# Optimization experiments

Measured on AMD Instinct MI355X. Metric: run time of the kernel, lower is better.

## Reference

```python
import jax, jax.numpy as jnp
import numpy as np

NUM_ELEMENTS = 14
EMPTY_ID, WALL_ID = 0, 1
# 8-neighborhood direction offsets (dy, dx); DIRS[(a+4)%8] == -DIRS[a]
DIRS = [(-1, 0), (-1, 1), (0, 1), (1, 1), (1, 0), (1, -1), (0, -1), (-1, -1)]


def shift(x, a):
    """out[..., i, j] = x[..., i+dy, j+dx] with zero padding at borders (pw.direction_func)."""
    dy, dx = DIRS[a]
    B, C, H, W = x.shape
    xp = jnp.pad(x, ((0, 0), (0, 0), (1, 1), (1, 1)))
    return jax.lax.slice(xp, (0, 0, 1 + dy, 1 + dx), (B, C, 1 + dy + H, 1 + dx + W))


def setup_inputs() -> dict:
    key = jax.random.key(0)
    k1, k2 = jax.random.split(key)
    B, C, H, W = 4, NUM_ELEMENTS + 6, 512, 512
    world = jax.random.uniform(k1, (B, C, H, W), dtype=jnp.float32)
    velocity_field = jax.random.normal(k2, (B, 2, H, W), dtype=jnp.float32)
    elem_empty = jnp.zeros((C,), dtype=jnp.float32).at[EMPTY_ID].set(1.0)
    return {"world": world, "velocity_field": velocity_field, "elem_empty": elem_empty}


def reference(world, velocity_field, elem_empty):
    dtype = world.dtype
    empty_vec = elem_empty[None, :, None, None]  # [1, C, 1, 1]
    inv_2pi = 1.0 / (2.0 * np.pi)

    for _ in range(2):
        mag = jnp.linalg.norm(velocity_field, axis=1, keepdims=True)  # [B,1,H,W]
        raw = inv_2pi * jnp.arccos(velocity_field[:, 1:2] / (mag + 0.001))
        ang = jnp.where(velocity_field[:, 0:1] < 0, 1.0 - raw, raw)
        bucket = jnp.mod(jnp.floor(ang * 8.0 + 0.5), 8.0)
        vel_enough = mag > 0.1
        vdelta = velocity_field
        for a in range(8):
            opp = (a + 4) % 8
            empty_b = world[:, EMPTY_ID:EMPTY_ID + 1] > 0.5
            wall_b = world[:, WALL_ID:WALL_ID + 1] > 0.5
            is_match = bucket == a
            is_empty_dir = shift(empty_b, a) & (~wall_b)
            sa = is_match & vel_enough & is_empty_dir          # does_become_empty
            sb = shift(sa, opp)                                 # does_become_opposite
            saf = sa.astype(dtype)
            sbf = sb.astype(dtype)
            opp_world = shift(world, opp)
            # interp_vel: world - sa*world - sb*world + sa*empty_vec + sb*opp_world
            world = world - saf * world - sbf * world + saf * empty_vec + sbf * opp_world
            opp_vel = shift(velocity_field, opp)
            vdelta = vdelta - saf * velocity_field * 0.5 + sbf * opp_vel * 0.5
        velocity_field = vdelta

    velocity_field = velocity_field * 0.95
    kernel = jnp.ones((1, 1, 3, 3), dtype) / 18.0

    def smooth(ch):  # ch: [B,1,H,W]
        conv = jax.lax.conv_general_dilated(
            ch, kernel, window_strides=(1, 1), padding=((1, 1), (1, 1)),
            dimension_numbers=("NCHW", "OIHW", "NCHW"))
        return conv + ch * 0.5

    velocity_field = jnp.concatenate(
        [smooth(velocity_field[:, 0:1]), smooth(velocity_field[:, 1:2])], axis=1)
    world = world.at[:, NUM_ELEMENTS + 4:NUM_ELEMENTS + 6].set(velocity_field)
    return world, velocity_field
```

## Files before the change

### kernel.cpp

```cpp
#include <hip/hip_runtime.h>
#include <math.h>

#define HH 512
#define WW 512
#define HW (HH*WW)
#define BATCH 4
#define NCH 18
#define BHW (BATCH*HW)

__device__ __constant__ int cDG[8] = {-512,-511,1,513,512,511,-1,-513};
__device__ __constant__ int cDT[8] = {-48,-47,1,49,48,47,-1,-49};

__global__ __launch_bounds__(256) void bv_bucket_kernel(
    const float* __restrict__ vel, unsigned char* __restrict__ bk,
    unsigned* __restrict__ pcount)
{
    int idx = blockIdx.x*256 + threadIdx.x;
    if (idx == 0) { pcount[0] = 0; pcount[1] = 0; }
    if (idx >= BHW) return;
    int b = idx >> 18;
    int rem = idx & (HW-1);
    const float* vb = vel + (size_t)b*2*HW;
    float vy = vb[rem];
    float vx = vb[HW + rem];
    float a2 = vy*vy;
    float b2 = vx*vx;
    float mag = sqrtf(a2 + b2);
    float xx = vx / (mag + 0.001f);
    float af = (float)acos((double)xx);
    const float inv2pi = (float)(1.0/(2.0*3.14159265358979323846));
    float raw = inv2pi * af;
    float ang = (vy < 0.0f) ? (1.0f - raw) : raw;
    float t = ang * 8.0f + 0.5f;
    int bkt = (int)floorf(t);
    bkt &= 7;
    unsigned char e = (mag > 0.1f) ? (unsigned char)8 : (unsigned char)0;
    bk[idx] = (unsigned char)(bkt | e);
}

#define ATP 48
#define ATC (48*48)
#define ANT 512
#define PAD 49

template<bool COMPOSE>
__global__ __launch_bounds__(ANT) void bv_mask_kernel(
    const float* __restrict__ Win, int Cin,
    float* __restrict__ Wout, int Cout,
    const unsigned char* __restrict__ bkall,
    unsigned char* __restrict__ Mg,
    unsigned char* __restrict__ SBg,
    int* __restrict__ SrcOut,
    const int* __restrict__ Src1g,
    unsigned* __restrict__ pcount,
    uint2* __restrict__ tlist,
    unsigned listcap,
    const float* __restrict__ elem_empty)
{
    __shared__ __align__(16) unsigned char SHM[40864];
    float* A0  = ((float*)(SHM +     0)) + PAD;
    float* A1  = ((float*)(SHM +  9608)) + PAD;
    float* B0F = ((float*)(SHM + 19216)) + PAD;
    float* B1F = ((float*)(SHM + 28824)) + PAD;
    unsigned char* KSH = SHM + 38432 + PAD;
    unsigned* sCnt = (unsigned*)(SHM + 40840);

    unsigned char* MSHb = SHM + 19216 + PAD;
    unsigned char* SBb  = SHM + 28824 + PAD;

    const int tid = threadIdx.x;
    const int blk = blockIdx.x;
    const int tx = blk & 15, ty = (blk >> 4) & 15, b = blk >> 8;
    const int x0 = tx*32 - 8, y0 = ty*32 - 8;

    const float* inb  = Win  + (size_t)b*Cin*HW;
    float*       outb = Wout + (size_t)b*Cout*HW;
    const unsigned char* bkb = bkall + ((size_t)b << 18);
    unsigned char* Mob  = Mg  + ((size_t)b << 18);
    unsigned char* SBob = SBg + ((size_t)b << 18);
    int*           Srb  = SrcOut + ((size_t)b << 18);

    const float e0 = elem_empty[0];
    const float e1 = elem_empty[1];

    float v0r[4], v1r[4];
    unsigned kreg[4], mreg[4];
    unsigned mtail = 0;

    if (tid == 0) sCnt[0] = 0;

    #pragma unroll
    for (int k = 0; k < 4; ++k) {
        int l = tid + (k << 9);
        int ly = l / ATP, lx = l - ly*ATP;
        int gy = y0 + ly, gx = x0 + lx;
        bool in = ((unsigned)gy < HH) && ((unsigned)gx < WW);
        int g = gy*WW + gx;
        float v0 = 0.f, v1 = 0.f; unsigned char kk = 0;
        if (in) { v0 = inb[g]; v1 = inb[HW + g]; kk = bkb[g]; }
        A0[l] = v0; A1[l] = v1; KSH[l] = kk;
        v0r[k] = v0; v1r[k] = v1; kreg[k] = kk; mreg[k] = 0;
    }
    if (tid < 256) {
        int l = 2048 + tid;
        int ly = l / ATP, lx = l - ly*ATP;
        int gy = y0 + ly, gx = x0 + lx;
        bool in = ((unsigned)gy < HH) && ((unsigned)gx < WW);
        int g = gy*WW + gx;
        float v0 = 0.f, v1 = 0.f; unsigned char kk = 0;
        if (in) { v0 = inb[g]; v1 = inb[HW + g]; kk = bkb[g]; }
        A0[l] = v0; A1[l] = v1; KSH[l] = kk;
    }
    __syncthreads();

    #pragma unroll
    for (int a = 0; a < 8; ++a) {
        const int doff = cDT[a];
        const unsigned tgt = (unsigned)(a | 8);
        const float* cA0 = (a & 1) ? B0F : A0;
        const float* cA1 = (a & 1) ? B1F : A1;
        float* nA0 = (a & 1) ? A0 : B0F;
        float* nA1 = (a & 1) ? A1 : B1F;
        #pragma unroll
        for (int k = 0; k < 4; ++k) {
            const int l = tid + (k << 9);
            const int ln = l + doff;
            const int lo = l - doff;
            float a0l = v0r[k], a1l = v1r[k];
            float a0n = cA0[ln];
            float a0o = cA0[lo], a1o = cA1[lo];
            unsigned ko = KSH[lo];
            bool sal = ((kreg[k] & 15u) == tgt) & (a0n > 0.5f) & !(a1l > 0.5f);
            bool sao = ((ko & 15u) == tgt) & (a0l > 0.5f) & !(a1o > 0.5f);
            mreg[k] |= (sal ? 1u : 0u) << a;
            float sa = sal ? 1.0f : 0.0f;
            float sb = sao ? 1.0f : 0.0f;
            float r0 = a0l - sa*a0l; r0 = r0 - sb*a0l; r0 = r0 + sa*e0; r0 = r0 + sb*a0o;
            float r1 = a1l - sa*a1l; r1 = r1 - sb*a1l; r1 = r1 + sa*e1; r1 = r1 + sb*a1o;
            v0r[k] = r0; v1r[k] = r1;
            nA0[l] = r0; nA1[l] = r1;
        }
        if (tid < 256) {
            const int l = 2048 + tid;
            const int ln = l + doff;
            const int lo = l - doff;
            float a0l = cA0[l], a1l = cA1[l];
            float a0n = cA0[ln];
            float a0o = cA0[lo], a1o = cA1[lo];
            unsigned kl = KSH[l], ko = KSH[lo];
            bool sal = ((kl & 15u) == tgt) & (a0n > 0.5f) & !(a1l > 0.5f);
            bool sao = ((ko & 15u) == tgt) & (a0l > 0.5f) & !(a1o > 0.5f);
            if (sal) mtail |= 1u << a;
            float sa = sal ? 1.0f : 0.0f;
            float sb = sao ? 1.0f : 0.0f;
            float r0 = a0l - sa*a0l; r0 = r0 - sb*a0l; r0 = r0 + sa*e0; r0 = r0 + sb*a0o;
            float r1 = a1l - sa*a1l; r1 = r1 - sb*a1l; r1 = r1 + sa*e1; r1 = r1 + sb*a1o;
            nA0[l] = r0; nA1[l] = r1;
        }
        __syncthreads();
    }

    #pragma unroll
    for (int k = 0; k < 4; ++k) MSHb[tid + (k << 9)] = (unsigned char)mreg[k];
    if (tid < 256) MSHb[2048 + tid] = (unsigned char)mtail;
    __syncthreads();

    for (int l = tid; l < ATC; l += ANT) {
        unsigned sb8 = 0;
        #pragma unroll
        for (int a = 0; a < 8; ++a) {
            int lo = l - cDT[a];
            sb8 |= (unsigned)((MSHb[lo] >> a) & 1) << a;
        }
        SBb[l] = (unsigned char)sb8;
    }
    __syncthreads();

    int tNeed[2]; unsigned tLL[2], tEy[2];
    #pragma unroll
    for (int it = 0; it < 2; ++it) {
        tNeed[it] = 0;
        int li = tid + (it << 9);
        int iy = li >> 5, ix = li & 31;
        int l = (iy + 8)*ATP + ix + 8;
        int gy = ty*32 + iy, gx = tx*32 + ix;
        int g = gy*WW + gx;
        outb[g]      = A0[l];
        outb[HW + g] = A1[l];
        unsigned mm = MSHb[l], sbb = SBb[l];
        Mob[g]  = (unsigned char)mm;
        SBob[g] = (unsigned char)sbb;

        int cc = l, ss = 7, kd = 0;
        unsigned m = mm, sb = sbb;
        while (true) {
            unsigned evt = (m | sb) & ((2u << ss) - 1u);
            if (!evt) { kd = 0; break; }
            int bb = 31 - __builtin_clz(evt);
            int ia = (m >> bb) & 1, ib = (sb >> bb) & 1;
            if (ia && ib) { kd = 2; break; }
            if (ia) { kd = 1; break; }
            cc -= cDT[bb]; ss = bb - 1;
            if (ss < 0) { kd = 0; break; }
            m = MSHb[cc]; sb = SBb[cc];
        }
        if (kd == 1) {
            Srb[g] = (int)(1u << 30);
        } else if (kd == 0) {
            int cly = cc / ATP, clx = cc - cly*ATP;
            unsigned s = (unsigned)((y0 + cly)*WW + (x0 + clx));
            if (!COMPOSE) {
                Srb[g] = (int)s;
            } else {
                unsigned r1 = (unsigned)Src1g[((size_t)b << 18) + s];
                unsigned k1 = r1 >> 30;
                if (k1 == 0u)      Srb[g] = (int)r1;
                else if (k1 == 1u) Srb[g] = (int)(1u << 30);
                else { tNeed[it] = 1; tEy[it] = s; }
            }
        } else {
            if (!COMPOSE) {
                Srb[g] = (int)(2u << 30);
            } else {
                int cly = cc / ATP, clx = cc - cly*ATP;
                unsigned ccg = (unsigned)((y0 + cly)*WW + (x0 + clx));
                tNeed[it] = 1;
                tEy[it] = (1u << 31) | ((unsigned)ss << 28) | ccg;
            }
        }
        if (COMPOSE && tNeed[it]) tLL[it] = atomicAdd(&sCnt[0], 1u);
    }
    if constexpr (COMPOSE) {
        __syncthreads();
        if (tid == 0) sCnt[1] = sCnt[0] ? atomicAdd(&pcount[1], sCnt[0]) : 0u;
        __syncthreads();
        unsigned lbase = sCnt[1];
        #pragma unroll
        for (int it = 0; it < 2; ++it) {
            if (!tNeed[it]) continue;
            int li = tid + (it << 9);
            int iy = li >> 5, ix = li & 31;
            int g = (ty*32 + iy)*WW + tx*32 + ix;
            unsigned lidx = lbase + tLL[it];
            if (lidx < listcap) {
                tlist[lidx] = make_uint2(((unsigned)b << 18) | (unsigned)g, tEy[it]);
                Srb[g] = (int)(2u << 30);
            } else {
                Srb[g] = (int)(3u << 30);
            }
        }
    }
}

__global__ __launch_bounds__(256) void bv_vdelta_kernel(
    const unsigned char* __restrict__ M,
    const unsigned char* __restrict__ SB,
    const float* __restrict__ vel,
    float* __restrict__ vdout,
    unsigned char* __restrict__ bkout,
    unsigned* __restrict__ pcount)
{
    int idx = blockIdx.x*256 + threadIdx.x;
    if (bkout && idx == 0) pcount[1] = 0;
    if (idx >= BHW) return;
    int b = idx >> 18;
    int g = idx & (HW-1);
    const float* velb = vel   + (size_t)b*2*HW;
    float*       vdb  = vdout + (size_t)b*2*HW;
    unsigned mm  = M[((size_t)b << 18) + g];
    unsigned sbb = SB[((size_t)b << 18) + g];
    float vy = velb[g], vx = velb[HW + g];
    float ddy = vy, ddx = vx;
    unsigned act = mm | sbb;
    if (act) {
        #pragma unroll
        for (int a = 0; a < 8; ++a) {
            if ((act >> a) & 1) {
                float sa = (float)((mm  >> a) & 1);
                float sb = (float)((sbb >> a) & 1);
                float voy = 0.f, vox = 0.f;
                if (sb != 0.f) {
                    int go = g - cDG[a];
                    voy = velb[go]; vox = velb[HW + go];
                }
                ddy = ddy - (sa*vy)*0.5f; ddy = ddy + (sb*voy)*0.5f;
                ddx = ddx - (sa*vx)*0.5f; ddx = ddx + (sb*vox)*0.5f;
            }
        }
    }
    vdb[g]      = ddy;
    vdb[HW + g] = ddx;
    if (bkout) {
        float a2 = ddy*ddy;
        float b2 = ddx*ddx;
        float mag = sqrtf(a2 + b2);
        float xx = ddx / (mag + 0.001f);
        float af = (float)acos((double)xx);
        const float inv2pi = (float)(1.0/(2.0*3.14159265358979323846));
        float raw = inv2pi * af;
        float ang = (ddy < 0.0f) ? (1.0f - raw) : raw;
        float t = ang * 8.0f + 0.5f;
        int bkt = (int)floorf(t);
        bkt &= 7;
        unsigned char e = (mag > 0.1f) ? (unsigned char)8 : (unsigned char)0;
        bkout[idx] = (unsigned char)(bkt | e);
    }
}

__device__ __attribute__((noinline)) float bv_eval(
    int cell, int stp,
    const unsigned char* __restrict__ M,
    const unsigned char* __restrict__ SB,
    const float* __restrict__ initc)
{
    float vstk[10]; int vsp = 0;
    int cs_cell[10], cs_stp[10], cs_ph[10]; int csp = 0;
    cs_cell[0] = cell; cs_stp[0] = stp; cs_ph[0] = 0; csp = 1;
    while (csp > 0) {
        int ph = cs_ph[csp-1];
        if (ph == 0) {
            int cc = cs_cell[csp-1], ss = cs_stp[csp-1];
            float result = 0.0f; int have = 0;
            while (true) {
                if (ss < 0) { result = initc[cc]; have = 1; break; }
                unsigned m = M[cc], sb = SB[cc];
                unsigned evt = (m | sb) & ((2u << ss) - 1u);
                if (!evt) { result = initc[cc]; have = 1; break; }
                int bb = 31 - __builtin_clz(evt);
                int ia = (m >> bb) & 1, ib = (sb >> bb) & 1;
                if (ia && ib) {
                    cs_cell[csp-1] = cc; cs_stp[csp-1] = bb; cs_ph[csp-1] = 1;
                    cs_cell[csp] = cc - cDG[bb]; cs_stp[csp] = bb - 1; cs_ph[csp] = 0; csp++;
                    break;
                }
                if (ia) { result = 0.0f; have = 1; break; }
                cc -= cDG[bb]; ss = bb - 1;
            }
            if (have) { vstk[vsp++] = result; csp--; }
        } else if (ph == 1) {
            cs_ph[csp-1] = 2;
            cs_cell[csp] = cs_cell[csp-1]; cs_stp[csp] = cs_stp[csp-1] - 1;
            cs_ph[csp] = 0; csp++;
        } else {
            float Bv = vstk[--vsp]; float Av = vstk[--vsp];
            vstk[vsp++] = Av - Bv;
            csp--;
        }
    }
    return vstk[0];
}

__device__ float bv_leaf1_1(int L,
    const unsigned char* __restrict__ M1,
    const unsigned char* __restrict__ SB1,
    const float* __restrict__ ic)
{
    int cc = L, ss = 7;
    while (true) {
        unsigned m = M1[cc], sb = SB1[cc];
        unsigned evt = (m | sb) & ((2u << ss) - 1u);
        if (!evt) break;
        int bb = 31 - __builtin_clz(evt);
        int ia = (m >> bb) & 1, ib = (sb >> bb) & 1;
        if (ia && ib) return bv_eval(cc, bb, M1, SB1, ic);
        if (ia) return 0.0f;
        cc -= cDG[bb]; ss = bb - 1;
        if (ss < 0) break;
    }
    return ic[cc];
}

__device__ float bv_eval1_ind(int cell, int stp,
    const unsigned char* __restrict__ M2,
    const unsigned char* __restrict__ SB2,
    const unsigned char* __restrict__ M1,
    const unsigned char* __restrict__ SB1,
    const float* __restrict__ ic)
{
    float vstk[10]; int vsp = 0;
    int cs_cell[10], cs_stp[10], cs_ph[10]; int csp = 0;
    cs_cell[0] = cell; cs_stp[0] = stp; cs_ph[0] = 0; csp = 1;
    while (csp > 0) {
        int ph = cs_ph[csp-1];
        if (ph == 0) {
            int cc = cs_cell[csp-1], ss = cs_stp[csp-1];
            int have = 0, zero = 0, leaf = 0;
            while (true) {
                if (ss < 0) { leaf = cc; have = 1; break; }
                unsigned m = M2[cc], sb = SB2[cc];
                unsigned evt = (m | sb) & ((2u << ss) - 1u);
                if (!evt) { leaf = cc; have = 1; break; }
                int bb = 31 - __builtin_clz(evt);
                int ia = (m >> bb) & 1, ib = (sb >> bb) & 1;
                if (ia && ib) {
                    cs_cell[csp-1] = cc; cs_stp[csp-1] = bb; cs_ph[csp-1] = 1;
                    cs_cell[csp] = cc - cDG[bb]; cs_stp[csp] = bb - 1; cs_ph[csp] = 0; csp++;
                    break;
                }
                if (ia) { zero = 1; have = 1; break; }
                cc -= cDG[bb]; ss = bb - 1;
            }
            if (have) {
                vstk[vsp++] = zero ? 0.0f : bv_leaf1_1(leaf, M1, SB1, ic);
                csp--;
            }
        } else if (ph == 1) {
            cs_ph[csp-1] = 2;
            cs_cell[csp] = cs_cell[csp-1]; cs_stp[csp] = cs_stp[csp-1] - 1;
            cs_ph[csp] = 0; csp++;
        } else {
            float Bv = vstk[--vsp]; float Av = vstk[--vsp];
            vstk[vsp++] = Av - Bv;
            csp--;
        }
    }
    return vstk[0];
}

__global__ __launch_bounds__(256) void bv_apply_kernel(
    const float* __restrict__ Win, int Cin,
    float* __restrict__ Wout, int Cout,
    const int* __restrict__ Src)
{
    int t = blockIdx.x*256 + threadIdx.x;
    if (t >= BHW/8) return;
    const int c0 = 2 + blockIdx.y*4;
    int p = t << 3;
    int b = p >> 18;
    int own = p & (HW-1);
    const float* inb  = Win  + (size_t)b*Cin*HW;
    float*       outb = Wout + (size_t)b*Cout*HW;
    const int* Srb = Src + ((size_t)b << 18);

    int4 sA = *(const int4*)(Srb + own);
    int4 sB = *(const int4*)(Srb + own + 4);
    unsigned sv[8] = {(unsigned)sA.x, (unsigned)sA.y, (unsigned)sA.z, (unsigned)sA.w,
                      (unsigned)sB.x, (unsigned)sB.y, (unsigned)sB.z, (unsigned)sB.w};
    int kind[8], idx[8]; bool need[8];
    bool allself = true;
    #pragma unroll
    for (int j = 0; j < 8; ++j) {
        kind[j] = (int)(sv[j] >> 30);
        idx[j]  = (int)(sv[j] & 0x3FFFFu);
        need[j] = (kind[j] != 0) || (idx[j] != own + j);
        allself = allself && !need[j];
    }

    if (allself) {
        #pragma unroll
        for (int c = 0; c < 4; ++c) {
            const float* ic = inb + (size_t)(c0 + c)*HW;
            float*       oc = outb + (size_t)(c0 + c)*HW;
            float4 va = *(const float4*)(ic + own);
            float4 vb = *(const float4*)(ic + own + 4);
            *(float4*)(oc + own)     = va;
            *(float4*)(oc + own + 4) = vb;
        }
        return;
    }
    #pragma unroll
    for (int c = 0; c < 4; ++c) {
        const float* ic = inb + (size_t)(c0 + c)*HW;
        float*       oc = outb + (size_t)(c0 + c)*HW;
        float4 va = *(const float4*)(ic + own);
        float4 vb = *(const float4*)(ic + own + 4);
        float r[8] = {va.x, va.y, va.z, va.w, vb.x, vb.y, vb.z, vb.w};
        #pragma unroll
        for (int j = 0; j < 8; ++j) {
            if (need[j])
                r[j] = (kind[j] == 0) ? ic[idx[j]] : 0.0f;
        }
        *(float4*)(oc + own)     = make_float4(r[0], r[1], r[2], r[3]);
        *(float4*)(oc + own + 4) = make_float4(r[4], r[5], r[6], r[7]);
    }
}

__global__ __launch_bounds__(256) void bv_tree_kernel(
    const float* __restrict__ Win,
    float* __restrict__ Wout,
    const uint2* __restrict__ tlist,
    const unsigned* __restrict__ pcount,
    unsigned listcap,
    const unsigned char* __restrict__ M1,
    const unsigned char* __restrict__ SB1,
    const unsigned char* __restrict__ M2,
    const unsigned char* __restrict__ SB2)
{
    unsigned n = pcount[1]; if (n > listcap) n = listcap;
    unsigned total = n * 16;
    for (unsigned i = blockIdx.x*256 + threadIdx.x; i < total; i += gridDim.x*256) {
        unsigned ei = i >> 4; int c = 2 + (int)(i & 15);
        uint2 e = tlist[ei];
        int b = (int)((e.x >> 18) & 3u);
        int g = (int)(e.x & 0x3FFFFu);
        const float* ic = Win  + (size_t)b*20*HW + (size_t)c*HW;
        float*       oc = Wout + (size_t)b*20*HW + (size_t)c*HW;
        const unsigned char* M1b  = M1  + ((size_t)b << 18);
        const unsigned char* SB1b = SB1 + ((size_t)b << 18);
        float r;
        if (e.y >> 31) {
            int cc = (int)(e.y & 0x3FFFFu);
            int ss = (int)((e.y >> 28) & 7u);
            const unsigned char* M2b  = M2  + ((size_t)b << 18);
            const unsigned char* SB2b = SB2 + ((size_t)b << 18);
            r = bv_eval1_ind(cc, ss, M2b, SB2b, M1b, SB1b, ic);
        } else {
            int s = (int)(e.y & 0x3FFFFu);
            r = bv_leaf1_1(s, M1b, SB1b, ic);
        }
        oc[g] = r;
    }
}

__global__ __launch_bounds__(256) void bv_smooth_kernel(
    const float* __restrict__ vin, float* __restrict__ dout)
{
    int idx = blockIdx.x*256 + threadIdx.x;
    if (idx >= BATCH*2*HW) return;
    int x = idx & (WW-1);
    int y = (idx >> 9) & (HH-1);
    int c = (idx >> 18) & 1;
    int b = idx >> 19;
    const float* vb = vin + (size_t)(b*2 + c)*HW;
    const float w18 = (float)(1.0/18.0);
    float acc = 0.0f;
    for (int ky = -1; ky <= 1; ++ky) {
        int yy = y + ky;
        if ((unsigned)yy >= HH) continue;
        for (int kx = -1; kx <= 1; ++kx) {
            int xx2 = x + kx;
            if ((unsigned)xx2 >= WW) continue;
            float s = 0.95f * vb[yy*WW + xx2];
            acc += s * w18;
        }
    }
    float sc = 0.95f * vb[y*WW + x];
    float res = acc + sc * 0.5f;
    dout[((size_t)b*20 + 18 + c)*HW + (size_t)(y<<9) + x] = res;
    dout[(size_t)BATCH*20*HW + (size_t)idx] = res;
}

extern "C" void kernel_launch(void* const* d_in, const int* in_sizes, int n_in,
                              void* d_out, int out_size, void* d_ws, size_t ws_size,
                              hipStream_t stream)
{
    const float* world_in   = (const float*)d_in[0];
    const float* vel_in     = (const float*)d_in[1];
    const float* elem_empty = (const float*)d_in[2];
    float* out = (float*)d_out;

    float* w01  = (float*)d_ws;
    float* vd1  = w01 + (size_t)BATCH*2*HW;
    float* vel2 = vd1 + (size_t)BATCH*2*HW;
    unsigned char* bk  = (unsigned char*)(vel2 + (size_t)BATCH*2*HW);
    unsigned char* M1  = bk  + (size_t)BHW;
    unsigned char* SB1 = M1  + (size_t)BHW;
    unsigned char* M2  = SB1 + (size_t)BHW;
    unsigned char* SB2 = M2  + (size_t)BHW;
    int* Src1 = (int*)(SB2 + (size_t)BHW);
    int* Src2 = Src1 + (size_t)BHW;
    unsigned* pcount = (unsigned*)(Src2 + (size_t)BHW);
    uint2* tlistb = (uint2*)(pcount + 16);
    const unsigned listcap = 1u << 18;

    dim3 blk(256);
    dim3 grd((BHW + 255)/256);
    dim3 g2((BATCH*2*HW + 255)/256);
    dim3 gA(BATCH*16*16);
    dim3 gB(BHW/8/256, 4);
    dim3 gT(1024);

    bv_bucket_kernel<<<grd, blk, 0, stream>>>(vel_in, bk, pcount);
    bv_mask_kernel<false><<<gA, dim3(ANT), 0, stream>>>(
        world_in, 20, w01, 2, bk, M1, SB1, Src1,
        (const int*)nullptr, pcount, (uint2*)nullptr, 0u, elem_empty);
    bv_vdelta_kernel<<<grd, blk, 0, stream>>>(M1, SB1, vel_in, vd1, bk, pcount);
    bv_mask_kernel<true><<<gA, dim3(ANT), 0, stream>>>(
        w01, 2, out, 20, bk, M2, SB2, Src2,
        Src1, pcount, tlistb, listcap, elem_empty);
    bv_vdelta_kernel<<<grd, blk, 0, stream>>>(M2, SB2, vd1, vel2,
                                              (unsigned char*)nullptr,
                                              (unsigned*)nullptr);
    bv_apply_kernel<<<gB, blk, 0, stream>>>(world_in, 20, out, 20, Src2);
    bv_tree_kernel<<<gT, blk, 0, stream>>>(world_in, out, tlistb, pcount,
                                           listcap, M1, SB1, M2, SB2);
    bv_smooth_kernel<<<g2, blk, 0, stream>>>(vel2, out);
}
```

Measured before the change: 174.7 us.

## Pack mask bytes into ushort and fuse apply and tree kernels

Interleaves the M and SB per-cell bitmasks into a single 16-bit array, so each consumer makes one load instead of two separate byte loads. Merges the apply and tree-walk kernels into one launch: grid row 4 runs the tree list while rows 0-3 do the apply. Apply now skips writing cells that the tree list owns, so the two parts do not race. Also drops noinline on bv_eval. The cost is scattered scalar stores when a group contains tree cells, and the tree-walk blocks now share the launch with the apply blocks.

```diff
diff --git a/kernel.cpp b/kernel.cpp
--- a/kernel.cpp
+++ b/kernel.cpp
@@ -48,8 +48,7 @@
     const float* __restrict__ Win, int Cin,
     float* __restrict__ Wout, int Cout,
     const unsigned char* __restrict__ bkall,
-    unsigned char* __restrict__ Mg,
-    unsigned char* __restrict__ SBg,
+    unsigned short* __restrict__ MSg,
     int* __restrict__ SrcOut,
     const int* __restrict__ Src1g,
     unsigned* __restrict__ pcount,
@@ -76,9 +75,8 @@
     const float* inb  = Win  + (size_t)b*Cin*HW;
     float*       outb = Wout + (size_t)b*Cout*HW;
     const unsigned char* bkb = bkall + ((size_t)b << 18);
-    unsigned char* Mob  = Mg  + ((size_t)b << 18);
-    unsigned char* SBob = SBg + ((size_t)b << 18);
-    int*           Srb  = SrcOut + ((size_t)b << 18);
+    unsigned short* MSob = MSg + ((size_t)b << 18);
+    int*            Srb  = SrcOut + ((size_t)b << 18);
 
     const float e0 = elem_empty[0];
     const float e1 = elem_empty[1];
@@ -188,8 +186,7 @@
         outb[g]      = A0[l];
         outb[HW + g] = A1[l];
         unsigned mm = MSHb[l], sbb = SBb[l];
-        Mob[g]  = (unsigned char)mm;
-        SBob[g] = (unsigned char)sbb;
+        MSob[g] = (unsigned short)(mm | (sbb << 8));
 
         int cc = l, ss = 7, kd = 0;
         unsigned m = mm, sb = sbb;
@@ -253,8 +250,7 @@
 }
 
 __global__ __launch_bounds__(256) void bv_vdelta_kernel(
-    const unsigned char* __restrict__ M,
-    const unsigned char* __restrict__ SB,
+    const unsigned short* __restrict__ MS,
     const float* __restrict__ vel,
     float* __restrict__ vdout,
     unsigned char* __restrict__ bkout,
@@ -267,8 +263,8 @@
     int g = idx & (HW-1);
     const float* velb = vel   + (size_t)b*2*HW;
     float*       vdb  = vdout + (size_t)b*2*HW;
-    unsigned mm  = M[((size_t)b << 18) + g];
-    unsigned sbb = SB[((size_t)b << 18) + g];
+    unsigned v = MS[((size_t)b << 18) + g];
+    unsigned mm = v & 255u, sbb = v >> 8;
     float vy = velb[g], vx = velb[HW + g];
     float ddy = vy, ddx = vx;
     unsigned act = mm | sbb;
@@ -307,10 +303,9 @@
     }
 }
 
-__device__ __attribute__((noinline)) float bv_eval(
+__device__ float bv_eval(
     int cell, int stp,
-    const unsigned char* __restrict__ M,
-    const unsigned char* __restrict__ SB,
+    const unsigned short* __restrict__ MS,
     const float* __restrict__ initc)
 {
     float vstk[10]; int vsp = 0;
@@ -323,7 +318,8 @@
             float result = 0.0f; int have = 0;
             while (true) {
                 if (ss < 0) { result = initc[cc]; have = 1; break; }
-                unsigned m = M[cc], sb = SB[cc];
+                unsigned v = MS[cc];
+                unsigned m = v & 255u, sb = v >> 8;
                 unsigned evt = (m | sb) & ((2u << ss) - 1u);
                 if (!evt) { result = initc[cc]; have = 1; break; }
                 int bb = 31 - __builtin_clz(evt);
@@ -351,18 +347,18 @@
 }
 
 __device__ float bv_leaf1_1(int L,
-    const unsigned char* __restrict__ M1,
-    const unsigned char* __restrict__ SB1,
+    const unsigned short* __restrict__ MS1,
     const float* __restrict__ ic)
 {
     int cc = L, ss = 7;
     while (true) {
-        unsigned m = M1[cc], sb = SB1[cc];
+        unsigned v = MS1[cc];
+        unsigned m = v & 255u, sb = v >> 8;
         unsigned evt = (m | sb) & ((2u << ss) - 1u);
         if (!evt) break;
         int bb = 31 - __builtin_clz(evt);
         int ia = (m >> bb) & 1, ib = (sb >> bb) & 1;
-        if (ia && ib) return bv_eval(cc, bb, M1, SB1, ic);
+        if (ia && ib) return bv_eval(cc, bb, MS1, ic);
         if (ia) return 0.0f;
         cc -= cDG[bb]; ss = bb - 1;
         if (ss < 0) break;
@@ -371,10 +367,8 @@
 }
 
 __device__ float bv_eval1_ind(int cell, int stp,
-    const unsigned char* __restrict__ M2,
-    const unsigned char* __restrict__ SB2,
-    const unsigned char* __restrict__ M1,
-    const unsigned char* __restrict__ SB1,
+    const unsigned short* __restrict__ MS2,
+    const unsigned short* __restrict__ MS1,
     const float* __restrict__ ic)
 {
     float vstk[10]; int vsp = 0;
@@ -387,7 +381,8 @@
             int have = 0, zero = 0, leaf = 0;
             while (true) {
                 if (ss < 0) { leaf = cc; have = 1; break; }
-                unsigned m = M2[cc], sb = SB2[cc];
+                unsigned v = MS2[cc];
+                unsigned m = v & 255u, sb = v >> 8;
                 unsigned evt = (m | sb) & ((2u << ss) - 1u);
                 if (!evt) { leaf = cc; have = 1; break; }
                 int bb = 31 - __builtin_clz(evt);
@@ -401,7 +396,7 @@
                 cc -= cDG[bb]; ss = bb - 1;
             }
             if (have) {
-                vstk[vsp++] = zero ? 0.0f : bv_leaf1_1(leaf, M1, SB1, ic);
+                vstk[vsp++] = zero ? 0.0f : bv_leaf1_1(leaf, MS1, ic);
                 csp--;
             }
         } else if (ph == 1) {
@@ -417,98 +412,98 @@
     return vstk[0];
 }
 
-__global__ __launch_bounds__(256) void bv_apply_kernel(
-    const float* __restrict__ Win, int Cin,
-    float* __restrict__ Wout, int Cout,
-    const int* __restrict__ Src)
-{
-    int t = blockIdx.x*256 + threadIdx.x;
-    if (t >= BHW/8) return;
-    const int c0 = 2 + blockIdx.y*4;
-    int p = t << 3;
-    int b = p >> 18;
-    int own = p & (HW-1);
-    const float* inb  = Win  + (size_t)b*Cin*HW;
-    float*       outb = Wout + (size_t)b*Cout*HW;
-    const int* Srb = Src + ((size_t)b << 18);
-
-    int4 sA = *(const int4*)(Srb + own);
-    int4 sB = *(const int4*)(Srb + own + 4);
-    unsigned sv[8] = {(unsigned)sA.x, (unsigned)sA.y, (unsigned)sA.z, (unsigned)sA.w,
-                      (unsigned)sB.x, (unsigned)sB.y, (unsigned)sB.z, (unsigned)sB.w};
-    int kind[8], idx[8]; bool need[8];
-    bool allself = true;
-    #pragma unroll
-    for (int j = 0; j < 8; ++j) {
-        kind[j] = (int)(sv[j] >> 30);
-        idx[j]  = (int)(sv[j] & 0x3FFFFu);
-        need[j] = (kind[j] != 0) || (idx[j] != own + j);
-        allself = allself && !need[j];
-    }
-
-    if (allself) {
+__global__ __launch_bounds__(256) void bv_apply_tree_kernel(
+    const float* __restrict__ Win,
+    float* __restrict__ Wout,
+    const int* __restrict__ Src,
+    const uint2* __restrict__ tlist,
+    const unsigned* __restrict__ pcount,
+    unsigned listcap,
+    const unsigned short* __restrict__ MS1,
+    const unsigned short* __restrict__ MS2)
+{
+    if (blockIdx.y < 4) {
+        int t = blockIdx.x*256 + threadIdx.x;
+        if (t >= BHW/8) return;
+        const int c0 = 2 + blockIdx.y*4;
+        int p = t << 3;
+        int b = p >> 18;
+        int own = p & (HW-1);
+        const float* inb  = Win  + (size_t)b*20*HW;
+        float*       outb = Wout + (size_t)b*20*HW;
+        const int* Srb = Src + ((size_t)b << 18);
+
+        int4 sA = *(const int4*)(Srb + own);
+        int4 sB = *(const int4*)(Srb + own + 4);
+        unsigned sv[8] = {(unsigned)sA.x, (unsigned)sA.y, (unsigned)sA.z, (unsigned)sA.w,
+                          (unsigned)sB.x, (unsigned)sB.y, (unsigned)sB.z, (unsigned)sB.w};
+        int kind[8], idx[8]; bool need[8];
+        bool allself = true, anyt = false;
+        #pragma unroll
+        for (int j = 0; j < 8; ++j) {
+            kind[j] = (int)(sv[j] >> 30);
+            idx[j]  = (int)(sv[j] & 0x3FFFFu);
+            need[j] = (kind[j] != 0) || (idx[j] != own + j);
+            allself = allself && !need[j];
+            anyt = anyt || (kind[j] == 2);
+        }
+
+        if (allself) {
+            #pragma unroll
+            for (int c = 0; c < 4; ++c) {
+                const float* ic = inb + (size_t)(c0 + c)*HW;
+                float*       oc = outb + (size_t)(c0 + c)*HW;
+                float4 va = *(const float4*)(ic + own);
+                float4 vb = *(const float4*)(ic + own + 4);
+                *(float4*)(oc + own)     = va;
+                *(float4*)(oc + own + 4) = vb;
+            }
+            return;
+        }
         #pragma unroll
         for (int c = 0; c < 4; ++c) {
             const float* ic = inb + (size_t)(c0 + c)*HW;
             float*       oc = outb + (size_t)(c0 + c)*HW;
             float4 va = *(const float4*)(ic + own);
             float4 vb = *(const float4*)(ic + own + 4);
-            *(float4*)(oc + own)     = va;
-            *(float4*)(oc + own + 4) = vb;
-        }
-        return;
-    }
-    #pragma unroll
-    for (int c = 0; c < 4; ++c) {
-        const float* ic = inb + (size_t)(c0 + c)*HW;
-        float*       oc = outb + (size_t)(c0 + c)*HW;
-        float4 va = *(const float4*)(ic + own);
-        float4 vb = *(const float4*)(ic + own + 4);
-        float r[8] = {va.x, va.y, va.z, va.w, vb.x, vb.y, vb.z, vb.w};
-        #pragma unroll
-        for (int j = 0; j < 8; ++j) {
-            if (need[j])
-                r[j] = (kind[j] == 0) ? ic[idx[j]] : 0.0f;
-        }
-        *(float4*)(oc + own)     = make_float4(r[0], r[1], r[2], r[3]);
-        *(float4*)(oc + own + 4) = make_float4(r[4], r[5], r[6], r[7]);
-    }
-}
-
-__global__ __launch_bounds__(256) void bv_tree_kernel(
-    const float* __restrict__ Win,
-    float* __restrict__ Wout,
-    const uint2* __restrict__ tlist,
-    const unsigned* __restrict__ pcount,
-    unsigned listcap,
-    const unsigned char* __restrict__ M1,
-    const unsigned char* __restrict__ SB1,
-    const unsigned char* __restrict__ M2,
-    const unsigned char* __restrict__ SB2)
-{
-    unsigned n = pcount[1]; if (n > listcap) n = listcap;
-    unsigned total = n * 16;
-    for (unsigned i = blockIdx.x*256 + threadIdx.x; i < total; i += gridDim.x*256) {
-        unsigned ei = i >> 4; int c = 2 + (int)(i & 15);
-        uint2 e = tlist[ei];
-        int b = (int)((e.x >> 18) & 3u);
-        int g = (int)(e.x & 0x3FFFFu);
-        const float* ic = Win  + (size_t)b*20*HW + (size_t)c*HW;
-        float*       oc = Wout + (size_t)b*20*HW + (size_t)c*HW;
-        const unsigned char* M1b  = M1  + ((size_t)b << 18);
-        const unsigned char* SB1b = SB1 + ((size_t)b << 18);
-        float r;
-        if (e.y >> 31) {
-            int cc = (int)(e.y & 0x3FFFFu);
-            int ss = (int)((e.y >> 28) & 7u);
-            const unsigned char* M2b  = M2  + ((size_t)b << 18);
-            const unsigned char* SB2b = SB2 + ((size_t)b << 18);
-            r = bv_eval1_ind(cc, ss, M2b, SB2b, M1b, SB1b, ic);
-        } else {
-            int s = (int)(e.y & 0x3FFFFu);
-            r = bv_leaf1_1(s, M1b, SB1b, ic);
-        }
-        oc[g] = r;
+            float r[8] = {va.x, va.y, va.z, va.w, vb.x, vb.y, vb.z, vb.w};
+            #pragma unroll
+            for (int j = 0; j < 8; ++j) {
+                if (need[j])
+                    r[j] = (kind[j] == 0) ? ic[idx[j]] : 0.0f;
+            }
+            if (!anyt) {
+                *(float4*)(oc + own)     = make_float4(r[0], r[1], r[2], r[3]);
+                *(float4*)(oc + own + 4) = make_float4(r[4], r[5], r[6], r[7]);
+            } else {
+                #pragma unroll
+                for (int j = 0; j < 8; ++j)
+                    if (kind[j] != 2) oc[own + j] = r[j];
+            }
+        }
+    } else {
+        unsigned n = pcount[1]; if (n > listcap) n = listcap;
+        unsigned total = n * 16;
+        for (unsigned i = blockIdx.x*256 + threadIdx.x; i < total; i += gridDim.x*256) {
+            unsigned ei = i >> 4; int c = 2 + (int)(i & 15);
+            uint2 e = tlist[ei];
+            int b = (int)((e.x >> 18) & 3u);
+            int g = (int)(e.x & 0x3FFFFu);
+            const float* ic = Win  + (size_t)b*20*HW + (size_t)c*HW;
+            float*       oc = Wout + (size_t)b*20*HW + (size_t)c*HW;
+            const unsigned short* MS1b = MS1 + ((size_t)b << 18);
+            float r;
+            if (e.y >> 31) {
+                int cc = (int)(e.y & 0x3FFFFu);
+                int ss = (int)((e.y >> 28) & 7u);
+                const unsigned short* MS2b = MS2 + ((size_t)b << 18);
+                r = bv_eval1_ind(cc, ss, MS2b, MS1b, ic);
+            } else {
+                int s = (int)(e.y & 0x3FFFFu);
+                r = bv_leaf1_1(s, MS1b, ic);
+            }
+            oc[g] = r;
+        }
     }
 }
 
@@ -553,11 +548,9 @@
     float* vd1  = w01 + (size_t)BATCH*2*HW;
     float* vel2 = vd1 + (size_t)BATCH*2*HW;
     unsigned char* bk  = (unsigned char*)(vel2 + (size_t)BATCH*2*HW);
-    unsigned char* M1  = bk  + (size_t)BHW;
-    unsigned char* SB1 = M1  + (size_t)BHW;
-    unsigned char* M2  = SB1 + (size_t)BHW;
-    unsigned char* SB2 = M2  + (size_t)BHW;
-    int* Src1 = (int*)(SB2 + (size_t)BHW);
+    unsigned short* MS1 = (unsigned short*)(bk + (size_t)BHW);
+    unsigned short* MS2 = MS1 + (size_t)BHW;
+    int* Src1 = (int*)(MS2 + (size_t)BHW);
     int* Src2 = Src1 + (size_t)BHW;
     unsigned* pcount = (unsigned*)(Src2 + (size_t)BHW);
     uint2* tlistb = (uint2*)(pcount + 16);
@@ -567,22 +560,21 @@
     dim3 grd((BHW + 255)/256);
     dim3 g2((BATCH*2*HW + 255)/256);
     dim3 gA(BATCH*16*16);
-    dim3 gB(BHW/8/256, 4);
-    dim3 gT(1024);
+    dim3 gF(BHW/8/256, 5);
 
     bv_bucket_kernel<<<grd, blk, 0, stream>>>(vel_in, bk, pcount);
     bv_mask_kernel<false><<<gA, dim3(ANT), 0, stream>>>(
-        world_in, 20, w01, 2, bk, M1, SB1, Src1,
+        world_in, 20, w01, 2, bk, MS1, Src1,
         (const int*)nullptr, pcount, (uint2*)nullptr, 0u, elem_empty);
-    bv_vdelta_kernel<<<grd, blk, 0, stream>>>(M1, SB1, vel_in, vd1, bk, pcount);
+    bv_vdelta_kernel<<<grd, blk, 0, stream>>>(MS1, vel_in, vd1, bk, pcount);
     bv_mask_kernel<true><<<gA, dim3(ANT), 0, stream>>>(
-        w01, 2, out, 20, bk, M2, SB2, Src2,
+        w01, 2, out, 20, bk, MS2, Src2,
         Src1, pcount, tlistb, listcap, elem_empty);
-    bv_vdelta_kernel<<<grd, blk, 0, stream>>>(M2, SB2, vd1, vel2,
+    bv_vdelta_kernel<<<grd, blk, 0, stream>>>(MS2, vd1, vel2,
                                               (unsigned char*)nullptr,
                                               (unsigned*)nullptr);
-    bv_apply_kernel<<<gB, blk, 0, stream>>>(world_in, 20, out, 20, Src2);
-    bv_tree_kernel<<<gT, blk, 0, stream>>>(world_in, out, tlistb, pcount,
-                                           listcap, M1, SB1, M2, SB2);
+    bv_apply_tree_kernel<<<gF, blk, 0, stream>>>(world_in, out, Src2,
+                                                 tlistb, pcount, listcap,
+                                                 MS1, MS2);
     bv_smooth_kernel<<<g2, blk, 0, stream>>>(vel2, out);
 }
```

After: 208.8 us. 19.5% more time.
